# Optimization experiments

Hardware: AMD Instinct MI355X
Metric: run time of the kernel (lower is better)

Reference implementation:

```python
import jax, jax.numpy as jnp
import numpy as np

D_MODEL = 1024
NUM_HEADS = 16
D_K = D_MODEL // NUM_HEADS
THETA = 10000.0
BATCH = 4
SEQ = 2048


def rope(x, positions, theta=THETA):
    # x: [B, H, S, d_k]; rotate interleaved pairs (x_{2i}, x_{2i+1})
    d_k = x.shape[-1]
    inv_freq = theta ** (-jnp.arange(0, d_k, 2, dtype=jnp.float32) / d_k)  # [d_k/2]
    ang = positions[:, None].astype(jnp.float32) * inv_freq[None, :]  # [S, d_k/2]
    cos, sin = jnp.cos(ang), jnp.sin(ang)
    x1 = x[..., 0::2]
    x2 = x[..., 1::2]
    r1 = x1 * cos - x2 * sin
    r2 = x1 * sin + x2 * cos
    out = jnp.stack([r1, r2], axis=-1).reshape(x.shape)
    return out.astype(x.dtype)


def setup_inputs() -> dict:
    key = jax.random.key(0)
    k0, k1, k2, k3, k4 = jax.random.split(key, 5)
    std_qk = 2.0 / (D_MODEL + D_MODEL)
    x = jax.random.normal(k0, (BATCH, SEQ, D_MODEL), dtype=jnp.float32)
    P_Q = jax.random.normal(k1, (D_MODEL, D_MODEL), dtype=jnp.float32) * std_qk
    P_K = jax.random.normal(k2, (D_MODEL, D_MODEL), dtype=jnp.float32) * std_qk
    P_V = jax.random.normal(k3, (D_MODEL, D_MODEL), dtype=jnp.float32) * std_qk
    P_O = jax.random.normal(k4, (D_MODEL, D_MODEL), dtype=jnp.float32) * std_qk
    return {"x": x, "P_Q": P_Q, "P_K": P_K, "P_V": P_V, "P_O": P_O}


def reference(x, P_Q, P_K, P_V, P_O):
    B, S, _ = x.shape
    positions = jnp.arange(S)

    def proj(P):
        y = jnp.einsum('bsd,ed->bse', x, P)  # e = num_heads*d_k
        return y.reshape(B, S, NUM_HEADS, D_K).transpose(0, 2, 1, 3)  # [B,H,S,d_k]

    Q = rope(proj(P_Q), positions)
    K = rope(proj(P_K), positions)
    V = proj(P_V)

    scores = jnp.einsum('bhqd,bhkd->bhqk', Q, K) / jnp.sqrt(jnp.asarray(D_K, x.dtype))
    causal = jnp.tril(jnp.ones((S, S), dtype=bool))
    scores = jnp.where(causal, scores, jnp.asarray(-jnp.inf, scores.dtype))
    attn = jax.nn.softmax(scores, axis=-1)
    out = jnp.einsum('bhqk,bhkd->bhqd', attn, V)  # [B,H,S,d_v]
    out = out.transpose(0, 2, 1, 3).reshape(B, S, NUM_HEADS * D_K)
    return jnp.einsum('bse,de->bsd', out, P_O)
```

## Files before the change

### kernel.cpp

```cpp
#include <hip/hip_runtime.h>

typedef unsigned short u16;
typedef unsigned int u32;
typedef float f32x4 __attribute__((ext_vector_type(4)));
typedef __bf16 bf16x8 __attribute__((ext_vector_type(8)));

#define S_LEN 2048
#define DMODEL 1024
#define NHEAD 16
#define DKH 64

__device__ __forceinline__ u16 f2bf(float f) {
    unsigned u = __float_as_uint(f);
    u += 0x7FFFu + ((u >> 16) & 1u);
    return (u16)(u >> 16);
}

__device__ __forceinline__ u32 pkbf2(float a, float b) {
#if __has_builtin(__builtin_amdgcn_cvt_pk_bf16_f32)
    typedef __bf16 bf16x2_t __attribute__((ext_vector_type(2)));
    bf16x2_t r = __builtin_amdgcn_cvt_pk_bf16_f32(a, b);
    u32 u; __builtin_memcpy(&u, &r, 4); return u;
#else
    return (u32)f2bf(a) | ((u32)f2bf(b) << 16);
#endif
}

#if __has_builtin(__builtin_amdgcn_exp2f)
#define EXP2(x) __builtin_amdgcn_exp2f(x)
#else
#define EXP2(x) exp2f(x)
#endif

__device__ __forceinline__ void lds_fence_wave() {
    __asm__ volatile("" ::: "memory");
    __builtin_amdgcn_s_waitcnt(0xC07F);
    __asm__ volatile("" ::: "memory");
}

__device__ __forceinline__ void glds16(const u16* g, u16* l) {
    __builtin_amdgcn_global_load_lds(
        (const __attribute__((address_space(1))) void*)(g),
        (__attribute__((address_space(3))) void*)(l), 16, 0, 0);
}

__global__ __launch_bounds__(256) void cvt_all(const float* __restrict__ x, const float* __restrict__ PQ,
                                               const float* __restrict__ PK, const float* __restrict__ PV,
                                               const float* __restrict__ PO,
                                               u16* __restrict__ xb, u16* __restrict__ Wqkv,
                                               u16* __restrict__ Wo) {
    int i = blockIdx.x * 256 + threadIdx.x;
    const float* src; u16* dst; int j;
    if (i < 2097152)      { src = x;  dst = xb;             j = i; }
    else if (i < 2359296) { src = PQ; dst = Wqkv;           j = i - 2097152; }
    else if (i < 2621440) { src = PK; dst = Wqkv + 1048576; j = i - 2359296; }
    else if (i < 2883584) { src = PV; dst = Wqkv + 2097152; j = i - 2621440; }
    else                  { src = PO; dst = Wo;             j = i - 2883584; }
    float4 v = reinterpret_cast<const float4*>(src)[j];
    uint2 o;
    o.x = pkbf2(v.x, v.y);
    o.y = pkbf2(v.z, v.w);
    reinterpret_cast<uint2*>(dst)[j] = o;
}

__device__ __forceinline__ void gemm_core(const u16* __restrict__ A, const u16* __restrict__ Bt,
                                          int K, int m0, int n0,
                                          u16* As, u16* Bs, f32x4 acc[4][4]) {
    const int tid  = threadIdx.x;
    const int lane = tid & 63;
    const int quad = lane >> 4, l15 = lane & 15;
    const int w    = tid >> 6;
    const int mq   = w & 1, nq = w >> 1;

    const int c0 = tid, c1 = tid + 256;
    const int r0 = c0 >> 2, k0 = ((c0 & 3) ^ ((r0 >> 1) & 3)) * 8;
    const int r1 = c1 >> 2, k1 = ((c1 & 3) ^ ((r1 >> 1) & 3)) * 8;
    const u16* ga0 = A  + (size_t)(m0 + r0) * K + k0;
    const u16* ga1 = A  + (size_t)(m0 + r1) * K + k1;
    const u16* gb0 = Bt + (size_t)(n0 + r0) * K + k0;
    const u16* gb1 = Bt + (size_t)(n0 + r1) * K + k1;

    const int swz = (quad ^ ((l15 >> 1) & 3)) * 8;

    auto stage = [&](int buf, int kk) {
        u16* ad = As + buf * 4096;
        u16* bd = Bs + buf * 4096;
        glds16(ga0 + kk, ad + c0 * 8);
        glds16(ga1 + kk, ad + c1 * 8);
        glds16(gb0 + kk, bd + c0 * 8);
        glds16(gb1 + kk, bd + c1 * 8);
    };

    stage(0, 0);
    for (int kk = 0; kk < K; kk += 32) {
        const int cur = (kk >> 5) & 1;
        __syncthreads();
        if (kk + 32 < K) stage(cur ^ 1, kk + 32);
        const u16* ra = As + cur * 4096 + (mq * 64 + l15) * 32 + swz;
        const u16* rb = Bs + cur * 4096 + (nq * 64 + l15) * 32 + swz;
        bf16x8 af[4], bfv[4];
#pragma unroll
        for (int t = 0; t < 4; ++t) {
            af[t]  = *reinterpret_cast<const bf16x8*>(ra + t * 512);
            bfv[t] = *reinterpret_cast<const bf16x8*>(rb + t * 512);
        }
#pragma unroll
        for (int mt = 0; mt < 4; ++mt)
#pragma unroll
            for (int nt = 0; nt < 4; ++nt)
                acc[mt][nt] = __builtin_amdgcn_mfma_f32_16x16x32_bf16(af[mt], bfv[nt], acc[mt][nt], 0, 0, 0);
    }
}

__global__ __launch_bounds__(256) void gemm_qkv_kernel(const u16* __restrict__ xb, const u16* __restrict__ Wqkv,
                                                       u16* __restrict__ Qb, u16* __restrict__ Kb,
                                                       u16* __restrict__ Vt) {
    __shared__ u16 As[2 * 128 * 32];
    __shared__ u16 Bs[2 * 128 * 32];
    f32x4 acc[4][4];
    const f32x4 zz = {0.f, 0.f, 0.f, 0.f};
#pragma unroll
    for (int i = 0; i < 4; ++i)
#pragma unroll
        for (int j = 0; j < 4; ++j) acc[i][j] = zz;

    const int m0 = blockIdx.y * 128;
    const int n0 = blockIdx.x * 128;
    gemm_core(xb, Wqkv, DMODEL, m0, n0, As, Bs, acc);

    const int lane = threadIdx.x & 63;
    const int quad = lane >> 4, l15 = lane & 15;
    const int w = threadIdx.x >> 6, mq = w & 1, nq = w >> 1;

#pragma unroll
    for (int nt = 0; nt < 4; ++nt) {
        const int ncol = n0 + nq*64 + nt*16 + l15;
        const int sel  = ncol >> 10;
        const int e    = ncol & 1023;
        const int h    = e >> 6, dk = e & 63;
#pragma unroll
        for (int mt = 0; mt < 4; ++mt) {
            const int mrow = m0 + mq*64 + mt*16 + quad*4;
            if (sel == 2) {
                int b = mrow >> 11, s = mrow & 2047;
                uint2 pv;
                pv.x = pkbf2(acc[mt][nt][0], acc[mt][nt][1]);
                pv.y = pkbf2(acc[mt][nt][2], acc[mt][nt][3]);
                *reinterpret_cast<uint2*>(&Vt[((size_t)(b * NHEAD + h) * DKH + dk) * S_LEN + s]) = pv;
            } else {
                float invf_rev = 0.15915494f * EXP2(-13.2877124f * (float)(dk & 62) * (1.0f / 64.0f));
                const float sc = sel ? 1.0f : 0.18033688f;
                u16* dst = sel ? Kb : Qb;
#pragma unroll
                for (int r = 0; r < 4; ++r) {
                    float val  = acc[mt][nt][r];
                    float part = __shfl_xor(val, 1);
                    int m = mrow + r;
                    int b = m >> 11, s = m & 2047;
                    float rev = (float)s * invf_rev;
                    float fr  = rev - floorf(rev);
#if __has_builtin(__builtin_amdgcn_sinf) && __has_builtin(__builtin_amdgcn_cosf)
                    float sn = __builtin_amdgcn_sinf(fr);
                    float cs = __builtin_amdgcn_cosf(fr);
#else
                    float sn, cs;
                    __sincosf(fr * 6.2831853f, &sn, &cs);
#endif
                    sn *= sc; cs *= sc;
                    float o = (dk & 1) ? (part * sn + val * cs)
                                       : (val * cs - part * sn);
                    dst[((size_t)(b * NHEAD + h) * S_LEN + s) * DKH + dk] = f2bf(o);
                }
            }
        }
    }
}

__global__ __launch_bounds__(256) void attn_kernel(const u16* __restrict__ Qb, const u16* __restrict__ Kb,
                                                   const u16* __restrict__ Vt, u16* __restrict__ A2) {
    __shared__ u16 Ks[2][64 * 64];
    __shared__ u16 Vs[2][64 * 64];
    __shared__ u16 Ps[4][32 * 64];

    const int tid  = threadIdx.x;
    const int lane = tid & 63, w = tid >> 6;
    const int quad = lane >> 4, l15 = lane & 15;
    const int bh   = blockIdx.x & 63;
    const int qb   = 15 - (blockIdx.x >> 6);
    const int b = bh >> 4, h = bh & 15;
    const int q0w = qb * 128 + w * 32;
    const int nkt = 2 * (qb + 1);
    const int sw7 = l15 & 7;
    const f32x4 zz = {0.f, 0.f, 0.f, 0.f};

    uint4 ob; ob.x = ob.y = ob.z = ob.w = 0x3F803F80u;
    bf16x8 ones; __builtin_memcpy(&ones, &ob, 16);

    bf16x8 qf[2][2];
#pragma unroll
    for (int qt2 = 0; qt2 < 2; ++qt2)
#pragma unroll
        for (int hh = 0; hh < 2; ++hh)
            qf[qt2][hh] = *reinterpret_cast<const bf16x8*>(
                Qb + ((size_t)bh * S_LEN + q0w + qt2 * 16 + l15) * DKH + hh * 32 + quad * 8);

    f32x4 ot[4][2], lacc[2];
#pragma unroll
    for (int mt = 0; mt < 4; ++mt) { ot[mt][0] = zz; ot[mt][1] = zz; }
    lacc[0] = zz; lacc[1] = zz;

    const int c0 = tid, c1 = tid + 256;
    const int r0 = c0 >> 3, kc0 = ((c0 & 7) ^ (r0 & 7)) * 8;
    const int r1 = c1 >> 3, kc1 = ((c1 & 7) ^ (r1 & 7)) * 8;
    const u16* gk0 = Kb + ((size_t)bh * S_LEN + r0) * DKH + kc0;
    const u16* gk1 = Kb + ((size_t)bh * S_LEN + r1) * DKH + kc1;
    const u16* gv0 = Vt + ((size_t)bh * DKH + r0) * S_LEN + kc0;
    const u16* gv1 = Vt + ((size_t)bh * DKH + r1) * S_LEN + kc1;
    u16* Pw = &Ps[w][0];
    u16* prow0 = Pw + l15 * 64 + (quad & 1) * 4;
    u16* prow1 = Pw + (16 + l15) * 64 + (quad & 1) * 4;

    auto stage = [&](u16* kdst, u16* vdst, int kt) {
        const size_t key0 = (size_t)kt * 64;
        glds16(gk0 + key0 * DKH, kdst + c0 * 8);
        glds16(gk1 + key0 * DKH, kdst + c1 * 8);
        glds16(gv0 + key0,       vdst + c0 * 8);
        glds16(gv1 + key0,       vdst + c1 * 8);
    };

    auto compute = [&](const u16* Kbuf, const u16* Vbuf, int key0) {
        f32x4 st[4][2];
#pragma unroll
        for (int kt4 = 0; kt4 < 4; ++kt4) {
            const u16* krow = Kbuf + (kt4 * 16 + l15) * 64;
            bf16x8 ka0 = *reinterpret_cast<const bf16x8*>(krow + (quad ^ sw7) * 8);
            bf16x8 ka1 = *reinterpret_cast<const bf16x8*>(krow + ((4 + quad) ^ sw7) * 8);
#pragma unroll
            for (int qt2 = 0; qt2 < 2; ++qt2) {
                f32x4 s = __builtin_amdgcn_mfma_f32_16x16x32_bf16(ka0, qf[qt2][0], zz, 0, 0, 0);
                st[kt4][qt2] = __builtin_amdgcn_mfma_f32_16x16x32_bf16(ka1, qf[qt2][1], s, 0, 0, 0);
            }
        }
        if (key0 + 63 > q0w) {
#pragma unroll
            for (int qt2 = 0; qt2 < 2; ++qt2) {
                const int qrow = q0w + qt2 * 16 + l15;
#pragma unroll
                for (int kt4 = 0; kt4 < 4; ++kt4) {
                    const int kbase = key0 + kt4 * 16 + quad * 4;
#pragma unroll
                    for (int r = 0; r < 4; ++r)
                        if (kbase + r > qrow) st[kt4][qt2][r] = -3.0e38f;
                }
            }
        }
#pragma unroll
        for (int qt2 = 0; qt2 < 2; ++qt2) {
            u16* prow = qt2 ? prow1 : prow0;
#pragma unroll
            for (int kt4 = 0; kt4 < 4; ++kt4) {
                uint2 pv;
                pv.x = pkbf2(EXP2(st[kt4][qt2][0]), EXP2(st[kt4][qt2][1]));
                pv.y = pkbf2(EXP2(st[kt4][qt2][2]), EXP2(st[kt4][qt2][3]));
                *reinterpret_cast<uint2*>(prow + ((2 * kt4 + (quad >> 1)) ^ sw7) * 8) = pv;
            }
        }
        lds_fence_wave();
        bf16x8 pb[2][2];
#pragma unroll
        for (int qt2 = 0; qt2 < 2; ++qt2)
#pragma unroll
            for (int kh = 0; kh < 2; ++kh)
                pb[qt2][kh] = *reinterpret_cast<const bf16x8*>(
                    Pw + (qt2 * 16 + l15) * 64 + ((kh * 4 + quad) ^ sw7) * 8);
#pragma unroll
        for (int mt = 0; mt < 4; ++mt) {
            const u16* vrow = Vbuf + (mt * 16 + l15) * 64;
            bf16x8 va0 = *reinterpret_cast<const bf16x8*>(vrow + (quad ^ sw7) * 8);
            bf16x8 va1 = *reinterpret_cast<const bf16x8*>(vrow + ((4 + quad) ^ sw7) * 8);
#pragma unroll
            for (int qt2 = 0; qt2 < 2; ++qt2) {
                ot[mt][qt2] = __builtin_amdgcn_mfma_f32_16x16x32_bf16(va0, pb[qt2][0], ot[mt][qt2], 0, 0, 0);
                ot[mt][qt2] = __builtin_amdgcn_mfma_f32_16x16x32_bf16(va1, pb[qt2][1], ot[mt][qt2], 0, 0, 0);
            }
        }
#pragma unroll
        for (int qt2 = 0; qt2 < 2; ++qt2) {
            lacc[qt2] = __builtin_amdgcn_mfma_f32_16x16x32_bf16(ones, pb[qt2][0], lacc[qt2], 0, 0, 0);
            lacc[qt2] = __builtin_amdgcn_mfma_f32_16x16x32_bf16(ones, pb[qt2][1], lacc[qt2], 0, 0, 0);
        }
    };

    stage(&Ks[0][0], &Vs[0][0], 0);
#pragma unroll 1
    for (int kt = 0; kt < nkt; kt += 2) {
        __syncthreads();
        stage(&Ks[1][0], &Vs[1][0], kt + 1);
        compute(&Ks[0][0], &Vs[0][0], kt * 64);
        __syncthreads();
        if (kt + 2 < nkt) stage(&Ks[0][0], &Vs[0][0], kt + 2);
        compute(&Ks[1][0], &Vs[1][0], (kt + 1) * 64);
    }

    lds_fence_wave();
#pragma unroll
    for (int qt2 = 0; qt2 < 2; ++qt2) {
        const float il = 1.0f / lacc[qt2][0];
        u16* prow = qt2 ? prow1 : prow0;
#pragma unroll
        for (int mt = 0; mt < 4; ++mt) {
            uint2 ov;
            ov.x = pkbf2(ot[mt][qt2][0] * il, ot[mt][qt2][1] * il);
            ov.y = pkbf2(ot[mt][qt2][2] * il, ot[mt][qt2][3] * il);
            *reinterpret_cast<uint2*>(prow + ((2 * mt + (quad >> 1)) ^ sw7) * 8) = ov;
        }
    }
    lds_fence_wave();
    const int r2 = lane >> 1, half = lane & 1;
    const u16* orow = Pw + r2 * 64;
    u16* gout = A2 + ((size_t)b * S_LEN + q0w + r2) * DMODEL + h * DKH + half * 32;
#pragma unroll
    for (int c = 0; c < 4; ++c) {
        uint4 val = *reinterpret_cast<const uint4*>(orow + (((half * 4 + c) ^ (r2 & 7))) * 8);
        *reinterpret_cast<uint4*>(gout + c * 8) = val;
    }
}

__global__ __launch_bounds__(256) void gemm_oproj_kernel(const u16* __restrict__ A2, const u16* __restrict__ Wo,
                                                         float* __restrict__ Cout) {
    __shared__ u16 As[2 * 128 * 32];
    __shared__ u16 Bs[2 * 128 * 32];
    f32x4 acc[4][4];
    const f32x4 zz = {0.f, 0.f, 0.f, 0.f};
#pragma unroll
    for (int i = 0; i < 4; ++i)
#pragma unroll
        for (int j = 0; j < 4; ++j) acc[i][j] = zz;

    const int m0 = blockIdx.y * 128;
    const int n0 = blockIdx.x * 128;
    gemm_core(A2, Wo, DMODEL, m0, n0, As, Bs, acc);

    const int lane = threadIdx.x & 63;
    const int quad = lane >> 4, l15 = lane & 15;
    const int w = threadIdx.x >> 6, mq = w & 1, nq = w >> 1;
#pragma unroll
    for (int nt = 0; nt < 4; ++nt) {
        const int ncol = n0 + nq*64 + nt*16 + l15;
#pragma unroll
        for (int mt = 0; mt < 4; ++mt) {
            const int mrow = m0 + mq*64 + mt*16 + quad*4;
#pragma unroll
            for (int r = 0; r < 4; ++r)
                Cout[(size_t)(mrow + r) * DMODEL + ncol] = acc[mt][nt][r];
        }
    }
}

extern "C" void kernel_launch(void* const* d_in, const int* in_sizes, int n_in,
                              void* d_out, int out_size, void* d_ws, size_t ws_size,
                              hipStream_t stream) {
    const float* x  = (const float*)d_in[0];
    const float* PQ = (const float*)d_in[1];
    const float* PK = (const float*)d_in[2];
    const float* PV = (const float*)d_in[3];
    const float* PO = (const float*)d_in[4];
    float* out = (float*)d_out;
    char* ws = (char*)d_ws;

    const size_t MB = 1u << 20;
    u16* xb   = (u16*)(ws + 0 * MB);
    u16* Wqkv = (u16*)(ws + 16 * MB);
    u16* Wo   = (u16*)(ws + 22 * MB);
    u16* Qb   = (u16*)(ws + 24 * MB);
    u16* Kb   = (u16*)(ws + 40 * MB);
    u16* Vt   = (u16*)(ws + 56 * MB);
    u16* A2   = (u16*)(ws + 72 * MB);

    cvt_all<<<dim3(12288), dim3(256), 0, stream>>>(x, PQ, PK, PV, PO, xb, Wqkv, Wo);

    gemm_qkv_kernel<<<dim3(24, 64), dim3(256), 0, stream>>>(xb, Wqkv, Qb, Kb, Vt);

    attn_kernel<<<dim3(1024), dim3(256), 0, stream>>>(Qb, Kb, Vt, A2);

    gemm_oproj_kernel<<<dim3(8, 64), dim3(256), 0, stream>>>(A2, Wo, out);
}
```

Baseline: 258.9 us.

## Enlarge attention query tile to 256 rows per block with causal skip

Each attention block now covers 256 query rows, with 64 per wave instead of 32, so every staged K/V tile is reused across twice as many queries. The grid halves to 512 blocks, with a heavy/light pairing of query blocks to balance the causal work. Waves skip key tiles that lie entirely above their causal diagonal, and masking plus exp/pack are fused per sub-tile to cut score register pressure. The cost is more accumulator registers (launch bounds set to 2 blocks per SM), fewer blocks, and waves that idle at barriers while others still compute.

```diff
diff --git a/kernel.cpp b/kernel.cpp
--- a/kernel.cpp
+++ b/kernel.cpp
@@ -176,38 +176,43 @@
     }
 }
 
-__global__ __launch_bounds__(256) void attn_kernel(const u16* __restrict__ Qb, const u16* __restrict__ Kb,
-                                                   const u16* __restrict__ Vt, u16* __restrict__ A2) {
+__global__ __launch_bounds__(256, 2) void attn_kernel(const u16* __restrict__ Qb, const u16* __restrict__ Kb,
+                                                      const u16* __restrict__ Vt, u16* __restrict__ A2) {
     __shared__ u16 Ks[2][64 * 64];
     __shared__ u16 Vs[2][64 * 64];
-    __shared__ u16 Ps[4][32 * 64];
+    __shared__ u16 Ps[4][64 * 64];
 
     const int tid  = threadIdx.x;
     const int lane = tid & 63, w = tid >> 6;
     const int quad = lane >> 4, l15 = lane & 15;
-    const int bh   = blockIdx.x & 63;
-    const int qb   = 15 - (blockIdx.x >> 6);
+    const int i    = blockIdx.x;
+    const int bh   = i & 63;
+    const int tq   = (i >> 6) & 3;
+    const int qblk = (i < 256) ? (7 - tq) : tq;
     const int b = bh >> 4, h = bh & 15;
-    const int q0w = qb * 128 + w * 32;
-    const int nkt = 2 * (qb + 1);
+    const int q0w = qblk * 256 + w * 64;
+    const int nkt = 4 * (qblk + 1);
     const int sw7 = l15 & 7;
     const f32x4 zz = {0.f, 0.f, 0.f, 0.f};
 
     uint4 ob; ob.x = ob.y = ob.z = ob.w = 0x3F803F80u;
     bf16x8 ones; __builtin_memcpy(&ones, &ob, 16);
 
-    bf16x8 qf[2][2];
-#pragma unroll
-    for (int qt2 = 0; qt2 < 2; ++qt2)
-#pragma unroll
-        for (int hh = 0; hh < 2; ++hh)
-            qf[qt2][hh] = *reinterpret_cast<const bf16x8*>(
-                Qb + ((size_t)bh * S_LEN + q0w + qt2 * 16 + l15) * DKH + hh * 32 + quad * 8);
-
-    f32x4 ot[4][2], lacc[2];
-#pragma unroll
-    for (int mt = 0; mt < 4; ++mt) { ot[mt][0] = zz; ot[mt][1] = zz; }
-    lacc[0] = zz; lacc[1] = zz;
+    bf16x8 qf[4][2];
+#pragma unroll
+    for (int qt = 0; qt < 4; ++qt)
+#pragma unroll
+        for (int kh = 0; kh < 2; ++kh)
+            qf[qt][kh] = *reinterpret_cast<const bf16x8*>(
+                Qb + ((size_t)bh * S_LEN + q0w + qt * 16 + l15) * DKH + kh * 32 + quad * 8);
+
+    f32x4 ot[4][4], lacc[4];
+#pragma unroll
+    for (int mt = 0; mt < 4; ++mt)
+#pragma unroll
+        for (int qt = 0; qt < 4; ++qt) ot[mt][qt] = zz;
+#pragma unroll
+    for (int qt = 0; qt < 4; ++qt) lacc[qt] = zz;
 
     const int c0 = tid, c1 = tid + 256;
     const int r0 = c0 >> 3, kc0 = ((c0 & 7) ^ (r0 & 7)) * 8;
@@ -217,8 +222,6 @@
     const u16* gv0 = Vt + ((size_t)bh * DKH + r0) * S_LEN + kc0;
     const u16* gv1 = Vt + ((size_t)bh * DKH + r1) * S_LEN + kc1;
     u16* Pw = &Ps[w][0];
-    u16* prow0 = Pw + l15 * 64 + (quad & 1) * 4;
-    u16* prow1 = Pw + (16 + l15) * 64 + (quad & 1) * 4;
 
     auto stage = [&](u16* kdst, u16* vdst, int kt) {
         const size_t key0 = (size_t)kt * 64;
@@ -229,65 +232,53 @@
     };
 
     auto compute = [&](const u16* Kbuf, const u16* Vbuf, int key0) {
-        f32x4 st[4][2];
+        const bool edge = (key0 + 63 > q0w + 63 - 192 + (3 - w) * 0) && (key0 + 63 > q0w);
 #pragma unroll
         for (int kt4 = 0; kt4 < 4; ++kt4) {
             const u16* krow = Kbuf + (kt4 * 16 + l15) * 64;
             bf16x8 ka0 = *reinterpret_cast<const bf16x8*>(krow + (quad ^ sw7) * 8);
             bf16x8 ka1 = *reinterpret_cast<const bf16x8*>(krow + ((4 + quad) ^ sw7) * 8);
 #pragma unroll
-            for (int qt2 = 0; qt2 < 2; ++qt2) {
-                f32x4 s = __builtin_amdgcn_mfma_f32_16x16x32_bf16(ka0, qf[qt2][0], zz, 0, 0, 0);
-                st[kt4][qt2] = __builtin_amdgcn_mfma_f32_16x16x32_bf16(ka1, qf[qt2][1], s, 0, 0, 0);
+            for (int qt = 0; qt < 4; ++qt) {
+                f32x4 s = __builtin_amdgcn_mfma_f32_16x16x32_bf16(ka0, qf[qt][0], zz, 0, 0, 0);
+                s = __builtin_amdgcn_mfma_f32_16x16x32_bf16(ka1, qf[qt][1], s, 0, 0, 0);
+                if (edge) {
+                    const int qrow = q0w + qt * 16 + l15;
+                    const int kbase = key0 + kt4 * 16 + quad * 4;
+#pragma unroll
+                    for (int r = 0; r < 4; ++r)
+                        if (kbase + r > qrow) s[r] = -3.0e38f;
+                }
+                uint2 pv;
+                pv.x = pkbf2(EXP2(s[0]), EXP2(s[1]));
+                pv.y = pkbf2(EXP2(s[2]), EXP2(s[3]));
+                *reinterpret_cast<uint2*>(Pw + (qt * 16 + l15) * 64 + (quad & 1) * 4 +
+                                          ((2 * kt4 + (quad >> 1)) ^ sw7) * 8) = pv;
             }
         }
-        if (key0 + 63 > q0w) {
-#pragma unroll
-            for (int qt2 = 0; qt2 < 2; ++qt2) {
-                const int qrow = q0w + qt2 * 16 + l15;
-#pragma unroll
-                for (int kt4 = 0; kt4 < 4; ++kt4) {
-                    const int kbase = key0 + kt4 * 16 + quad * 4;
-#pragma unroll
-                    for (int r = 0; r < 4; ++r)
-                        if (kbase + r > qrow) st[kt4][qt2][r] = -3.0e38f;
-                }
-            }
-        }
-#pragma unroll
-        for (int qt2 = 0; qt2 < 2; ++qt2) {
-            u16* prow = qt2 ? prow1 : prow0;
-#pragma unroll
-            for (int kt4 = 0; kt4 < 4; ++kt4) {
-                uint2 pv;
-                pv.x = pkbf2(EXP2(st[kt4][qt2][0]), EXP2(st[kt4][qt2][1]));
-                pv.y = pkbf2(EXP2(st[kt4][qt2][2]), EXP2(st[kt4][qt2][3]));
-                *reinterpret_cast<uint2*>(prow + ((2 * kt4 + (quad >> 1)) ^ sw7) * 8) = pv;
-            }
-        }
         lds_fence_wave();
-        bf16x8 pb[2][2];
-#pragma unroll
-        for (int qt2 = 0; qt2 < 2; ++qt2)
+        bf16x8 pb[4][2];
+#pragma unroll
+        for (int qt = 0; qt < 4; ++qt)
 #pragma unroll
             for (int kh = 0; kh < 2; ++kh)
-                pb[qt2][kh] = *reinterpret_cast<const bf16x8*>(
-                    Pw + (qt2 * 16 + l15) * 64 + ((kh * 4 + quad) ^ sw7) * 8);
+                pb[qt][kh] = *reinterpret_cast<const bf16x8*>(
+                    Pw + (qt * 16 + l15) * 64 + ((kh * 4 + quad) ^ sw7) * 8);
+#pragma unroll
+        for (int qt = 0; qt < 4; ++qt) {
+            lacc[qt] = __builtin_amdgcn_mfma_f32_16x16x32_bf16(ones, pb[qt][0], lacc[qt], 0, 0, 0);
+            lacc[qt] = __builtin_amdgcn_mfma_f32_16x16x32_bf16(ones, pb[qt][1], lacc[qt], 0, 0, 0);
+        }
 #pragma unroll
         for (int mt = 0; mt < 4; ++mt) {
             const u16* vrow = Vbuf + (mt * 16 + l15) * 64;
             bf16x8 va0 = *reinterpret_cast<const bf16x8*>(vrow + (quad ^ sw7) * 8);
             bf16x8 va1 = *reinterpret_cast<const bf16x8*>(vrow + ((4 + quad) ^ sw7) * 8);
 #pragma unroll
-            for (int qt2 = 0; qt2 < 2; ++qt2) {
-                ot[mt][qt2] = __builtin_amdgcn_mfma_f32_16x16x32_bf16(va0, pb[qt2][0], ot[mt][qt2], 0, 0, 0);
-                ot[mt][qt2] = __builtin_amdgcn_mfma_f32_16x16x32_bf16(va1, pb[qt2][1], ot[mt][qt2], 0, 0, 0);
+            for (int qt = 0; qt < 4; ++qt) {
+                ot[mt][qt] = __builtin_amdgcn_mfma_f32_16x16x32_bf16(va0, pb[qt][0], ot[mt][qt], 0, 0, 0);
+                ot[mt][qt] = __builtin_amdgcn_mfma_f32_16x16x32_bf16(va1, pb[qt][1], ot[mt][qt], 0, 0, 0);
             }
-        }
-#pragma unroll
-        for (int qt2 = 0; qt2 < 2; ++qt2) {
-            lacc[qt2] = __builtin_amdgcn_mfma_f32_16x16x32_bf16(ones, pb[qt2][0], lacc[qt2], 0, 0, 0);
-            lacc[qt2] = __builtin_amdgcn_mfma_f32_16x16x32_bf16(ones, pb[qt2][1], lacc[qt2], 0, 0, 0);
         }
     };
 
@@ -296,33 +287,37 @@
     for (int kt = 0; kt < nkt; kt += 2) {
         __syncthreads();
         stage(&Ks[1][0], &Vs[1][0], kt + 1);
-        compute(&Ks[0][0], &Vs[0][0], kt * 64);
+        if (kt * 64 <= q0w + 63) compute(&Ks[0][0], &Vs[0][0], kt * 64);
         __syncthreads();
         if (kt + 2 < nkt) stage(&Ks[0][0], &Vs[0][0], kt + 2);
-        compute(&Ks[1][0], &Vs[1][0], (kt + 1) * 64);
+        if ((kt + 1) * 64 <= q0w + 63) compute(&Ks[1][0], &Vs[1][0], (kt + 1) * 64);
     }
 
     lds_fence_wave();
 #pragma unroll
-    for (int qt2 = 0; qt2 < 2; ++qt2) {
-        const float il = 1.0f / lacc[qt2][0];
-        u16* prow = qt2 ? prow1 : prow0;
+    for (int qt = 0; qt < 4; ++qt) {
+        const float il = 1.0f / lacc[qt][0];
+        u16* prow = Pw + (qt * 16 + l15) * 64 + (quad & 1) * 4;
 #pragma unroll
         for (int mt = 0; mt < 4; ++mt) {
             uint2 ov;
-            ov.x = pkbf2(ot[mt][qt2][0] * il, ot[mt][qt2][1] * il);
-            ov.y = pkbf2(ot[mt][qt2][2] * il, ot[mt][qt2][3] * il);
+            ov.x = pkbf2(ot[mt][qt][0] * il, ot[mt][qt][1] * il);
+            ov.y = pkbf2(ot[mt][qt][2] * il, ot[mt][qt][3] * il);
             *reinterpret_cast<uint2*>(prow + ((2 * mt + (quad >> 1)) ^ sw7) * 8) = ov;
         }
     }
     lds_fence_wave();
-    const int r2 = lane >> 1, half = lane & 1;
-    const u16* orow = Pw + r2 * 64;
-    u16* gout = A2 + ((size_t)b * S_LEN + q0w + r2) * DMODEL + h * DKH + half * 32;
-#pragma unroll
-    for (int c = 0; c < 4; ++c) {
-        uint4 val = *reinterpret_cast<const uint4*>(orow + (((half * 4 + c) ^ (r2 & 7))) * 8);
-        *reinterpret_cast<uint4*>(gout + c * 8) = val;
+    const int half = lane & 1;
+#pragma unroll
+    for (int rr = 0; rr < 2; ++rr) {
+        const int r2 = rr * 32 + (lane >> 1);
+        const u16* orow = Pw + r2 * 64;
+        u16* gout = A2 + ((size_t)b * S_LEN + q0w + r2) * DMODEL + h * DKH + half * 32;
+#pragma unroll
+        for (int c = 0; c < 4; ++c) {
+            uint4 val = *reinterpret_cast<const uint4*>(orow + (((half * 4 + c) ^ (r2 & 7))) * 8);
+            *reinterpret_cast<uint4*>(gout + c * 8) = val;
+        }
     }
 }
 
@@ -381,7 +376,7 @@
 
     gemm_qkv_kernel<<<dim3(24, 64), dim3(256), 0, stream>>>(xb, Wqkv, Qb, Kb, Vt);
 
-    attn_kernel<<<dim3(1024), dim3(256), 0, stream>>>(Qb, Kb, Vt, A2);
+    attn_kernel<<<dim3(512), dim3(256), 0, stream>>>(Qb, Kb, Vt, A2);
 
     gemm_oproj_kernel<<<dim3(8, 64), dim3(256), 0, stream>>>(A2, Wo, out);
 }
```

Result: slower. 266.0 us (+2.8%).
